# Performance work log

Hardware: AMD Instinct MI355X
Metric: run time of the kernel (lower is better)

Reference implementation:

```python
import jax, jax.numpy as jnp
import numpy as np

N_NODES = 100000


def gcn_conv(x, src, dst, W, b, n):
    # GCNConv: out = D^-1/2 (A + I) D^-1/2 (x @ W) + b, self-loops included in src/dst
    deg = jax.ops.segment_sum(jnp.ones_like(src, dtype=x.dtype), dst, num_segments=n)
    dinv = jnp.where(deg > 0, jax.lax.rsqrt(deg), 0.0)
    norm = dinv[src] * dinv[dst]                      # [E+N]
    h = x @ W                                         # [N, out] small GEMM first (PyG flow)
    msg = h[src] * norm[:, None]                      # gather + scale
    out = jax.ops.segment_sum(msg, dst, num_segments=n)
    return out + b


def setup_inputs() -> dict:
    key = jax.random.key(0)
    k1, k2, k3, k4 = jax.random.split(key, 4)
    F_IN, H, C, E = 128, 16, 4, 3200000
    x = jax.random.normal(k1, (N_NODES, F_IN), dtype=jnp.float32)
    edge_index = jax.random.randint(k2, (2, E), 0, N_NODES, dtype=jnp.int64)
    W1 = jax.random.normal(k3, (F_IN, H), dtype=jnp.float32) * (1.0 / np.sqrt(F_IN))
    b1 = jnp.zeros((H,), dtype=jnp.float32)
    W2 = jax.random.normal(k4, (H, C), dtype=jnp.float32) * (1.0 / np.sqrt(H))
    b2 = jnp.zeros((C,), dtype=jnp.float32)
    return {"x": x, "edge_index": edge_index, "W1": W1, "b1": b1, "W2": W2, "b2": b2}


def reference(x, edge_index, W1, b1, W2, b2):
    n = x.shape[0]
    loop = jnp.arange(n, dtype=edge_index.dtype)
    src = jnp.concatenate([edge_index[0], loop])
    dst = jnp.concatenate([edge_index[1], loop])
    h = gcn_conv(x, src, dst, W1, b1, n)
    h = jax.nn.relu(h)
    # dropout is identity in eval mode
    h = gcn_conv(h, src, dst, W2, b2, n)
    return jax.nn.log_softmax(h, axis=1)
```

## Files before the change

### kernel.cpp

```cpp
#include <hip/hip_runtime.h>
#include <stdint.h>

#define F_IN 128
#define HDIM 16
#define CDIM 4

__global__ void k_detect(const int* __restrict__ w, int* __restrict__ flag) {
    __shared__ int s_any;
    if (threadIdx.x == 0) s_any = 0;
    __syncthreads();
    int nz = 0;
    for (int k = threadIdx.x; k < 1024; k += blockDim.x) nz |= w[2 * k + 1];
    if (nz) atomicOr(&s_any, 1);
    __syncthreads();
    if (threadIdx.x == 0) *flag = (s_any == 0) ? 1 : 0;
}

__global__ void k_zero_deg(int* __restrict__ deg_i, int n) {
    int i = blockIdx.x * blockDim.x + threadIdx.x;
    if (i < n) deg_i[i] = 0;
}

__global__ __launch_bounds__(256) void k_hist(const void* __restrict__ ei,
                                              const int* __restrict__ flag,
                                              int* __restrict__ deg_i, int E) {
    int e = blockIdx.x * blockDim.x + threadIdx.x;
    if (e >= E) return;
    int d;
    if (*flag) d = (int)((const long long*)ei)[E + e];
    else       d = ((const int*)ei)[E + e];
    atomicAdd(&deg_i[d], 1);
}

__global__ __launch_bounds__(256) void k_scan1(const int* __restrict__ deg_i,
                                               int* __restrict__ row_ptr,
                                               int* __restrict__ part, int n) {
    __shared__ int sd[256];
    int base = blockIdx.x * 1024, t = threadIdx.x;
    int v[4], ssum = 0;
#pragma unroll
    for (int k = 0; k < 4; ++k) {
        int i = base + t * 4 + k;
        v[k] = (i < n) ? deg_i[i] : 0;
        ssum += v[k];
    }
    sd[t] = ssum;
    __syncthreads();
    for (int off = 1; off < 256; off <<= 1) {
        int x = (t >= off) ? sd[t - off] : 0;
        __syncthreads();
        sd[t] += x;
        __syncthreads();
    }
    if (t == 255) part[blockIdx.x] = sd[255];
    int run = sd[t] - ssum;
#pragma unroll
    for (int k = 0; k < 4; ++k) {
        int i = base + t * 4 + k;
        if (i < n) row_ptr[i] = run;
        run += v[k];
    }
}

__global__ void k_scan2(int* __restrict__ part, int nb) {
    __shared__ int sd[128];
    int t = threadIdx.x;
    int own = (t < nb) ? part[t] : 0;
    sd[t] = own;
    __syncthreads();
    for (int off = 1; off < 128; off <<= 1) {
        int x = (t >= off) ? sd[t - off] : 0;
        __syncthreads();
        sd[t] += x;
        __syncthreads();
    }
    if (t < nb) part[t] = sd[t] - own;
}

__global__ void k_scan3(int* __restrict__ row_ptr, int* __restrict__ cursor,
                        const int* __restrict__ part, int n, int E) {
    int i = blockIdx.x * blockDim.x + threadIdx.x;
    if (i < n) {
        int r = row_ptr[i] + part[i >> 10];
        row_ptr[i] = r;
        cursor[i] = r;
    }
    if (i == 0) row_ptr[n] = E;
}

__global__ void k_rsqrt(const int* __restrict__ deg_i, float* __restrict__ dinv,
                        int n) {
    int i = blockIdx.x * blockDim.x + threadIdx.x;
    if (i < n) dinv[i] = rsqrtf((float)(deg_i[i] + 1));
}

__global__ __launch_bounds__(256) void k_scatter(const void* __restrict__ ei,
                                                 const int* __restrict__ flag,
                                                 int* __restrict__ cursor,
                                                 int* __restrict__ csr_src, int E) {
    int e = blockIdx.x * blockDim.x + threadIdx.x;
    if (e >= E) return;
    int s, d;
    if (*flag) {
        const long long* q = (const long long*)ei;
        s = (int)q[e]; d = (int)q[E + e];
    } else {
        const int* q = (const int*)ei;
        s = q[e]; d = q[E + e];
    }
    int pos = atomicAdd(&cursor[d], 1);
    csr_src[pos] = s;
}

__global__ __launch_bounds__(256) void k_gemm1(const float* __restrict__ x,
                                               const float* __restrict__ W1,
                                               const float* __restrict__ dinv,
                                               float* __restrict__ h1s, int n) {
    __shared__ float sW[F_IN * HDIM];
    __shared__ float sX[16][F_IN + 4];
    for (int i = threadIdx.x; i < F_IN * HDIM; i += 256) sW[i] = W1[i];
    int row0 = blockIdx.x * 16;
    const float4* x4 = (const float4*)(x + (size_t)row0 * F_IN);
    for (int i = threadIdx.x; i < 512; i += 256) {
        int r = i >> 5, c4 = i & 31;
        if (row0 + r < n) *(float4*)&sX[r][c4 * 4] = x4[i];
    }
    __syncthreads();
    int c = threadIdx.x & 15, r = threadIdx.x >> 4;
    float acc = 0.f;
#pragma unroll
    for (int k = 0; k < F_IN; ++k) acc += sX[r][k] * sW[k * HDIM + c];
    int row = row0 + r;
    if (row < n) h1s[(size_t)row * HDIM + c] = acc * dinv[row];
}

__global__ __launch_bounds__(256) void k_agg1f(const int* __restrict__ row_ptr,
                                               const int* __restrict__ csr_src,
                                               const float* __restrict__ h1s,
                                               const float* __restrict__ dinv,
                                               const float* __restrict__ b1,
                                               const float* __restrict__ W2,
                                               float* __restrict__ h2s, int n) {
    int node = blockIdx.x * 4 + (threadIdx.x >> 6);
    if (node >= n) return;
    int lane = threadIdx.x & 63;
    int f = lane & 15, slot = lane >> 4;
    int start = row_ptr[node], end = row_ptr[node + 1];
    float acc = 0.f;
    for (int j = start + slot; j < end; j += 4)
        acc += h1s[(size_t)csr_src[j] * HDIM + f];
    acc += __shfl_xor(acc, 16, 64);
    acc += __shfl_xor(acc, 32, 64);
    float di = dinv[node];
    float t = fmaxf(di * (acc + h1s[(size_t)node * HDIM + f]) + b1[f], 0.f);
    float4 w2 = ((const float4*)W2)[f];
    float a0 = t * w2.x, a1 = t * w2.y, a2 = t * w2.z, a3 = t * w2.w;
#pragma unroll
    for (int m = 1; m < 16; m <<= 1) {
        a0 += __shfl_xor(a0, m, 64);
        a1 += __shfl_xor(a1, m, 64);
        a2 += __shfl_xor(a2, m, 64);
        a3 += __shfl_xor(a3, m, 64);
    }
    if (lane == 0)
        ((float4*)h2s)[node] = make_float4(a0 * di, a1 * di, a2 * di, a3 * di);
}

__global__ __launch_bounds__(256) void k_agg2f(const int* __restrict__ row_ptr,
                                               const int* __restrict__ csr_src,
                                               const float* __restrict__ h2s,
                                               const float* __restrict__ dinv,
                                               const float* __restrict__ b2,
                                               float* __restrict__ out, int n) {
    int node = blockIdx.x * 4 + (threadIdx.x >> 6);
    if (node >= n) return;
    int lane = threadIdx.x & 63;
    int c = lane & 3, slot = lane >> 2;
    int start = row_ptr[node], end = row_ptr[node + 1];
    float acc = 0.f;
    for (int j = start + slot; j < end; j += 16)
        acc += h2s[(size_t)csr_src[j] * CDIM + c];
#pragma unroll
    for (int m = 4; m < 64; m <<= 1) acc += __shfl_xor(acc, m, 64);
    float z = dinv[node] * (acc + h2s[(size_t)node * CDIM + c]) + b2[c];
    float mx = fmaxf(z, __shfl_xor(z, 1, 64));
    mx = fmaxf(mx, __shfl_xor(mx, 2, 64));
    float ex = __expf(z - mx);
    float ssum = ex + __shfl_xor(ex, 1, 64);
    ssum += __shfl_xor(ssum, 2, 64);
    if (lane < 4) out[(size_t)node * CDIM + c] = z - mx - __logf(ssum);
}

extern "C" void kernel_launch(void* const* d_in, const int* in_sizes, int n_in,
                              void* d_out, int out_size, void* d_ws, size_t ws_size,
                              hipStream_t stream) {
    const float* x  = (const float*)d_in[0];
    const void*  ei = d_in[1];
    const float* W1 = (const float*)d_in[2];
    const float* b1 = (const float*)d_in[3];
    const float* W2 = (const float*)d_in[4];
    const float* b2 = (const float*)d_in[5];
    float* out = (float*)d_out;

    int n = in_sizes[0] / F_IN;
    int E = in_sizes[1] / 2;

    char* ws = (char*)d_ws;
    size_t off = 0;
    auto alloc = [&](size_t bytes) {
        char* p = ws + off;
        off = (off + bytes + 255) & ~(size_t)255;
        return p;
    };
    int*   flag    = (int*)alloc(256);
    int*   deg_i   = (int*)alloc((size_t)n * 4);
    float* dinv    = (float*)alloc((size_t)n * 4);
    int*   row_ptr = (int*)alloc((size_t)(n + 1) * 4);
    int*   cursor  = (int*)alloc((size_t)n * 4);
    int*   part    = (int*)alloc(512 * 4);
    float* h1s     = (float*)alloc((size_t)n * HDIM * 4);
    float* h2s     = (float*)alloc((size_t)n * CDIM * 4);
    int*   csr_src = (int*)alloc((size_t)E * 4);
    (void)ws_size;

    int nb = (n + 1023) / 1024;

    hipLaunchKernelGGL(k_detect, dim3(1), dim3(256), 0, stream, (const int*)ei, flag);
    hipLaunchKernelGGL(k_zero_deg, dim3((n + 255) / 256), dim3(256), 0, stream,
                       deg_i, n);
    hipLaunchKernelGGL(k_hist, dim3((E + 255) / 256), dim3(256), 0, stream,
                       ei, flag, deg_i, E);
    hipLaunchKernelGGL(k_scan1, dim3(nb), dim3(256), 0, stream,
                       deg_i, row_ptr, part, n);
    hipLaunchKernelGGL(k_scan2, dim3(1), dim3(128), 0, stream, part, nb);
    hipLaunchKernelGGL(k_scan3, dim3((n + 255) / 256), dim3(256), 0, stream,
                       row_ptr, cursor, part, n, E);
    hipLaunchKernelGGL(k_rsqrt, dim3((n + 255) / 256), dim3(256), 0, stream,
                       deg_i, dinv, n);
    hipLaunchKernelGGL(k_gemm1, dim3((n + 15) / 16), dim3(256), 0, stream,
                       x, W1, dinv, h1s, n);
    hipLaunchKernelGGL(k_scatter, dim3((E + 255) / 256), dim3(256), 0, stream,
                       ei, flag, cursor, csr_src, E);
    hipLaunchKernelGGL(k_agg1f, dim3((n + 3) / 4), dim3(256), 0, stream,
                       row_ptr, csr_src, h1s, dinv, b1, W2, h2s, n);
    hipLaunchKernelGGL(k_agg2f, dim3((n + 3) / 4), dim3(256), 0, stream,
                       row_ptr, csr_src, h2s, dinv, b2, out, n);
}
```

Baseline: 616.0 us.

## Replace per-node CSR build with coarse bucketed edge sort and shared-memory aggregation

Drops the full per-node CSR construction (global atomic histogram, three-kernel scan, per-edge global atomic scatter). Edges are instead bucketed by destination into groups of 256 nodes, using block-local histograms and tile-level reservation of output ranges. Each edge is packed as source plus a local destination offset. Degree and both aggregation passes then run one block per bucket and accumulate into shared-memory slabs with LDS atomics, which cuts global atomic traffic and kernel count. The trade-off is heavy LDS atomic contention in the aggregation kernels, only about 391 blocks per aggregation launch, and packing limits that assume n below 131072 and at most 512 buckets.

Result: no change. 604.9 us (-1.8%).

```diff
diff --git a/kernel.cpp b/kernel.cpp
--- a/kernel.cpp
+++ b/kernel.cpp
@@ -4,6 +4,10 @@
 #define F_IN 128
 #define HDIM 16
 #define CDIM 4
+#define BSH  8
+#define BNODES 256
+#define SMASK 131071
+#define TILE 8192
 
 __global__ void k_detect(const int* __restrict__ w, int* __restrict__ flag) {
     __shared__ int s_any;
@@ -16,100 +20,104 @@
     if (threadIdx.x == 0) *flag = (s_any == 0) ? 1 : 0;
 }
 
-__global__ void k_zero_deg(int* __restrict__ deg_i, int n) {
-    int i = blockIdx.x * blockDim.x + threadIdx.x;
-    if (i < n) deg_i[i] = 0;
-}
-
-__global__ __launch_bounds__(256) void k_hist(const void* __restrict__ ei,
-                                              const int* __restrict__ flag,
-                                              int* __restrict__ deg_i, int E) {
-    int e = blockIdx.x * blockDim.x + threadIdx.x;
-    if (e >= E) return;
-    int d;
-    if (*flag) d = (int)((const long long*)ei)[E + e];
-    else       d = ((const int*)ei)[E + e];
-    atomicAdd(&deg_i[d], 1);
-}
-
-__global__ __launch_bounds__(256) void k_scan1(const int* __restrict__ deg_i,
-                                               int* __restrict__ row_ptr,
-                                               int* __restrict__ part, int n) {
-    __shared__ int sd[256];
-    int base = blockIdx.x * 1024, t = threadIdx.x;
-    int v[4], ssum = 0;
-#pragma unroll
-    for (int k = 0; k < 4; ++k) {
-        int i = base + t * 4 + k;
-        v[k] = (i < n) ? deg_i[i] : 0;
-        ssum += v[k];
-    }
-    sd[t] = ssum;
-    __syncthreads();
-    for (int off = 1; off < 256; off <<= 1) {
+__global__ void k_zero(int* __restrict__ bcnt) {
+    bcnt[threadIdx.x] = 0;
+}
+
+__global__ __launch_bounds__(256) void k_bhist(const void* __restrict__ ei,
+                                               const int* __restrict__ flag,
+                                               int* __restrict__ bcnt,
+                                               int E, int nbuk) {
+    __shared__ int h[512];
+    for (int b = threadIdx.x; b < 512; b += 256) h[b] = 0;
+    __syncthreads();
+    int stride = gridDim.x * 256;
+    bool f64 = (*flag != 0);
+    for (int e = blockIdx.x * 256 + threadIdx.x; e < E; e += stride) {
+        int d = f64 ? (int)((const long long*)ei)[E + e] : ((const int*)ei)[E + e];
+        atomicAdd(&h[d >> BSH], 1);
+    }
+    __syncthreads();
+    for (int b = threadIdx.x; b < nbuk; b += 256)
+        if (h[b]) atomicAdd(&bcnt[b], h[b]);
+}
+
+__global__ __launch_bounds__(512) void k_bscan(const int* __restrict__ bcnt,
+                                               int* __restrict__ bbase,
+                                               int* __restrict__ bcur,
+                                               int nbuk, int E) {
+    __shared__ int sd[512];
+    int t = threadIdx.x;
+    int own = (t < nbuk) ? bcnt[t] : 0;
+    sd[t] = own;
+    __syncthreads();
+    for (int off = 1; off < 512; off <<= 1) {
         int x = (t >= off) ? sd[t - off] : 0;
         __syncthreads();
         sd[t] += x;
         __syncthreads();
     }
-    if (t == 255) part[blockIdx.x] = sd[255];
-    int run = sd[t] - ssum;
-#pragma unroll
-    for (int k = 0; k < 4; ++k) {
-        int i = base + t * 4 + k;
-        if (i < n) row_ptr[i] = run;
-        run += v[k];
-    }
-}
-
-__global__ void k_scan2(int* __restrict__ part, int nb) {
-    __shared__ int sd[128];
-    int t = threadIdx.x;
-    int own = (t < nb) ? part[t] : 0;
-    sd[t] = own;
-    __syncthreads();
-    for (int off = 1; off < 128; off <<= 1) {
-        int x = (t >= off) ? sd[t - off] : 0;
-        __syncthreads();
-        sd[t] += x;
-        __syncthreads();
-    }
-    if (t < nb) part[t] = sd[t] - own;
-}
-
-__global__ void k_scan3(int* __restrict__ row_ptr, int* __restrict__ cursor,
-                        const int* __restrict__ part, int n, int E) {
-    int i = blockIdx.x * blockDim.x + threadIdx.x;
-    if (i < n) {
-        int r = row_ptr[i] + part[i >> 10];
-        row_ptr[i] = r;
-        cursor[i] = r;
-    }
-    if (i == 0) row_ptr[n] = E;
-}
-
-__global__ void k_rsqrt(const int* __restrict__ deg_i, float* __restrict__ dinv,
-                        int n) {
-    int i = blockIdx.x * blockDim.x + threadIdx.x;
-    if (i < n) dinv[i] = rsqrtf((float)(deg_i[i] + 1));
-}
-
-__global__ __launch_bounds__(256) void k_scatter(const void* __restrict__ ei,
-                                                 const int* __restrict__ flag,
-                                                 int* __restrict__ cursor,
-                                                 int* __restrict__ csr_src, int E) {
-    int e = blockIdx.x * blockDim.x + threadIdx.x;
-    if (e >= E) return;
-    int s, d;
-    if (*flag) {
-        const long long* q = (const long long*)ei;
-        s = (int)q[e]; d = (int)q[E + e];
-    } else {
-        const int* q = (const int*)ei;
-        s = q[e]; d = q[E + e];
-    }
-    int pos = atomicAdd(&cursor[d], 1);
-    csr_src[pos] = s;
+    if (t < nbuk) { int ex = sd[t] - own; bbase[t] = ex; bcur[t] = ex; }
+    if (t == 0) bbase[nbuk] = E;
+}
+
+__global__ __launch_bounds__(512) void k_bscatter(const void* __restrict__ ei,
+                                                  const int* __restrict__ flag,
+                                                  int* __restrict__ bcur,
+                                                  int* __restrict__ bpk,
+                                                  int E, int nbuk) {
+    __shared__ int hist[512], loff[512], rbase[512];
+    __shared__ int lpk[TILE];
+    __shared__ unsigned short lb[TILE];
+    int tid = threadIdx.x;
+    int tstart = blockIdx.x * TILE;
+    int cnt = min(TILE, E - tstart);
+    for (int b = tid; b < 512; b += 512) { hist[b] = 0; loff[b] = 0; }
+    __syncthreads();
+    bool f64 = (*flag != 0);
+    for (int k = 0; k < TILE / 512; ++k) {
+        int i = tid + k * 512;
+        if (i < cnt) {
+            int e = tstart + i, s, d;
+            if (f64) {
+                const long long* q = (const long long*)ei;
+                s = (int)q[e]; d = (int)q[E + e];
+            } else {
+                const int* q = (const int*)ei;
+                s = q[e]; d = q[E + e];
+            }
+            int b = d >> BSH;
+            lpk[i] = s | ((d & (BNODES - 1)) << 17);
+            lb[i] = (unsigned short)b;
+            atomicAdd(&hist[b], 1);
+        }
+    }
+    __syncthreads();
+    if (tid < nbuk && hist[tid] > 0) rbase[tid] = atomicAdd(&bcur[tid], hist[tid]);
+    __syncthreads();
+    for (int k = 0; k < TILE / 512; ++k) {
+        int i = tid + k * 512;
+        if (i < cnt) {
+            int b = lb[i];
+            int p = rbase[b] + atomicAdd(&loff[b], 1);
+            bpk[p] = lpk[i];
+        }
+    }
+}
+
+__global__ __launch_bounds__(256) void k_bdeg(const int* __restrict__ bbase,
+                                              const int* __restrict__ bpk,
+                                              float* __restrict__ dinv, int n) {
+    __shared__ int cnt[BNODES];
+    int b = blockIdx.x, tid = threadIdx.x;
+    cnt[tid] = 0;
+    __syncthreads();
+    int start = bbase[b], end = bbase[b + 1];
+    for (int i = start + tid; i < end; i += 256)
+        atomicAdd(&cnt[bpk[i] >> 17], 1);
+    __syncthreads();
+    int g = b * BNODES + tid;
+    if (g < n) dinv[g] = rsqrtf((float)(cnt[tid] + 1));
 }
 
 __global__ __launch_bounds__(256) void k_gemm1(const float* __restrict__ x,
@@ -134,61 +142,91 @@
     if (row < n) h1s[(size_t)row * HDIM + c] = acc * dinv[row];
 }
 
-__global__ __launch_bounds__(256) void k_agg1f(const int* __restrict__ row_ptr,
-                                               const int* __restrict__ csr_src,
+__global__ __launch_bounds__(512) void k_bagg1(const int* __restrict__ bbase,
+                                               const int* __restrict__ bpk,
                                                const float* __restrict__ h1s,
                                                const float* __restrict__ dinv,
                                                const float* __restrict__ b1,
                                                const float* __restrict__ W2,
                                                float* __restrict__ h2s, int n) {
-    int node = blockIdx.x * 4 + (threadIdx.x >> 6);
-    if (node >= n) return;
-    int lane = threadIdx.x & 63;
-    int f = lane & 15, slot = lane >> 4;
-    int start = row_ptr[node], end = row_ptr[node + 1];
-    float acc = 0.f;
-    for (int j = start + slot; j < end; j += 4)
-        acc += h1s[(size_t)csr_src[j] * HDIM + f];
-    acc += __shfl_xor(acc, 16, 64);
-    acc += __shfl_xor(acc, 32, 64);
-    float di = dinv[node];
-    float t = fmaxf(di * (acc + h1s[(size_t)node * HDIM + f]) + b1[f], 0.f);
-    float4 w2 = ((const float4*)W2)[f];
-    float a0 = t * w2.x, a1 = t * w2.y, a2 = t * w2.z, a3 = t * w2.w;
+    __shared__ float slab[BNODES * HDIM];
+    int b = blockIdx.x, tid = threadIdx.x;
+    for (int j = tid; j < BNODES * HDIM; j += 512) slab[j] = 0.f;
+    __syncthreads();
+    int start = bbase[b], end = bbase[b + 1];
+    int f = tid & 15;
+    int i = start + (tid >> 4);
+    for (; i + 32 < end; i += 64) {
+        int e0 = bpk[i], e1 = bpk[i + 32];
+        float v0 = h1s[(size_t)(e0 & SMASK) * HDIM + f];
+        float v1 = h1s[(size_t)(e1 & SMASK) * HDIM + f];
+        atomicAdd(&slab[(e0 >> 17) * HDIM + f], v0);
+        atomicAdd(&slab[(e1 >> 17) * HDIM + f], v1);
+    }
+    for (; i < end; i += 32) {
+        int e0 = bpk[i];
+        float v0 = h1s[(size_t)(e0 & SMASK) * HDIM + f];
+        atomicAdd(&slab[(e0 >> 17) * HDIM + f], v0);
+    }
+    __syncthreads();
+    if (tid < BNODES) {
+        int g = b * BNODES + tid;
+        if (g < n) {
+            float di = dinv[g];
+            float a0 = 0.f, a1 = 0.f, a2 = 0.f, a3 = 0.f;
 #pragma unroll
-    for (int m = 1; m < 16; m <<= 1) {
-        a0 += __shfl_xor(a0, m, 64);
-        a1 += __shfl_xor(a1, m, 64);
-        a2 += __shfl_xor(a2, m, 64);
-        a3 += __shfl_xor(a3, m, 64);
-    }
-    if (lane == 0)
-        ((float4*)h2s)[node] = make_float4(a0 * di, a1 * di, a2 * di, a3 * di);
-}
-
-__global__ __launch_bounds__(256) void k_agg2f(const int* __restrict__ row_ptr,
-                                               const int* __restrict__ csr_src,
+            for (int j = 0; j < HDIM; ++j) {
+                float t = fmaxf(di * (slab[tid * HDIM + j] +
+                                      h1s[(size_t)g * HDIM + j]) + b1[j], 0.f);
+                float4 w2 = ((const float4*)W2)[j];
+                a0 += t * w2.x; a1 += t * w2.y; a2 += t * w2.z; a3 += t * w2.w;
+            }
+            ((float4*)h2s)[g] = make_float4(a0 * di, a1 * di, a2 * di, a3 * di);
+        }
+    }
+}
+
+__global__ __launch_bounds__(512) void k_bagg2(const int* __restrict__ bbase,
+                                               const int* __restrict__ bpk,
                                                const float* __restrict__ h2s,
                                                const float* __restrict__ dinv,
                                                const float* __restrict__ b2,
                                                float* __restrict__ out, int n) {
-    int node = blockIdx.x * 4 + (threadIdx.x >> 6);
-    if (node >= n) return;
-    int lane = threadIdx.x & 63;
-    int c = lane & 3, slot = lane >> 2;
-    int start = row_ptr[node], end = row_ptr[node + 1];
-    float acc = 0.f;
-    for (int j = start + slot; j < end; j += 16)
-        acc += h2s[(size_t)csr_src[j] * CDIM + c];
-#pragma unroll
-    for (int m = 4; m < 64; m <<= 1) acc += __shfl_xor(acc, m, 64);
-    float z = dinv[node] * (acc + h2s[(size_t)node * CDIM + c]) + b2[c];
-    float mx = fmaxf(z, __shfl_xor(z, 1, 64));
-    mx = fmaxf(mx, __shfl_xor(mx, 2, 64));
-    float ex = __expf(z - mx);
-    float ssum = ex + __shfl_xor(ex, 1, 64);
-    ssum += __shfl_xor(ssum, 2, 64);
-    if (lane < 4) out[(size_t)node * CDIM + c] = z - mx - __logf(ssum);
+    __shared__ float slab[BNODES * CDIM];
+    int b = blockIdx.x, tid = threadIdx.x;
+    for (int j = tid; j < BNODES * CDIM; j += 512) slab[j] = 0.f;
+    __syncthreads();
+    int start = bbase[b], end = bbase[b + 1];
+    int c = tid & 3;
+    int i = start + (tid >> 2);
+    for (; i + 128 < end; i += 256) {
+        int e0 = bpk[i], e1 = bpk[i + 128];
+        float v0 = h2s[(size_t)(e0 & SMASK) * CDIM + c];
+        float v1 = h2s[(size_t)(e1 & SMASK) * CDIM + c];
+        atomicAdd(&slab[(e0 >> 17) * CDIM + c], v0);
+        atomicAdd(&slab[(e1 >> 17) * CDIM + c], v1);
+    }
+    for (; i < end; i += 128) {
+        int e0 = bpk[i];
+        float v0 = h2s[(size_t)(e0 & SMASK) * CDIM + c];
+        atomicAdd(&slab[(e0 >> 17) * CDIM + c], v0);
+    }
+    __syncthreads();
+    if (tid < BNODES) {
+        int g = b * BNODES + tid;
+        if (g < n) {
+            float di = dinv[g];
+            float4 hs = ((const float4*)h2s)[g];
+            float z0 = di * (slab[tid * 4 + 0] + hs.x) + b2[0];
+            float z1 = di * (slab[tid * 4 + 1] + hs.y) + b2[1];
+            float z2 = di * (slab[tid * 4 + 2] + hs.z) + b2[2];
+            float z3 = di * (slab[tid * 4 + 3] + hs.w) + b2[3];
+            float m = fmaxf(fmaxf(z0, z1), fmaxf(z2, z3));
+            float s = expf(z0 - m) + expf(z1 - m) + expf(z2 - m) + expf(z3 - m);
+            float l = m + logf(s);
+            ((float4*)out)[g] = make_float4(z0 - l, z1 - l, z2 - l, z3 - l);
+        }
+    }
 }
 
 extern "C" void kernel_launch(void* const* d_in, const int* in_sizes, int n_in,
@@ -204,6 +242,7 @@
 
     int n = in_sizes[0] / F_IN;
     int E = in_sizes[1] / 2;
+    int nbuk = (n + BNODES - 1) >> BSH;
 
     char* ws = (char*)d_ws;
     size_t off = 0;
@@ -212,37 +251,31 @@
         off = (off + bytes + 255) & ~(size_t)255;
         return p;
     };
-    int*   flag    = (int*)alloc(256);
-    int*   deg_i   = (int*)alloc((size_t)n * 4);
-    float* dinv    = (float*)alloc((size_t)n * 4);
-    int*   row_ptr = (int*)alloc((size_t)(n + 1) * 4);
-    int*   cursor  = (int*)alloc((size_t)n * 4);
-    int*   part    = (int*)alloc(512 * 4);
-    float* h1s     = (float*)alloc((size_t)n * HDIM * 4);
-    float* h2s     = (float*)alloc((size_t)n * CDIM * 4);
-    int*   csr_src = (int*)alloc((size_t)E * 4);
+    int*   flag  = (int*)alloc(256);
+    int*   bcnt  = (int*)alloc(512 * 4);
+    int*   bbase = (int*)alloc(513 * 4);
+    int*   bcur  = (int*)alloc(512 * 4);
+    float* dinv  = (float*)alloc((size_t)n * 4);
+    float* h1s   = (float*)alloc((size_t)n * HDIM * 4);
+    float* h2s   = (float*)alloc((size_t)n * CDIM * 4);
+    int*   bpk   = (int*)alloc((size_t)E * 4);
     (void)ws_size;
 
-    int nb = (n + 1023) / 1024;
+    int ntiles = (E + TILE - 1) / TILE;
 
     hipLaunchKernelGGL(k_detect, dim3(1), dim3(256), 0, stream, (const int*)ei, flag);
-    hipLaunchKernelGGL(k_zero_deg, dim3((n + 255) / 256), dim3(256), 0, stream,
-                       deg_i, n);
-    hipLaunchKernelGGL(k_hist, dim3((E + 255) / 256), dim3(256), 0, stream,
-                       ei, flag, deg_i, E);
-    hipLaunchKernelGGL(k_scan1, dim3(nb), dim3(256), 0, stream,
-                       deg_i, row_ptr, part, n);
-    hipLaunchKernelGGL(k_scan2, dim3(1), dim3(128), 0, stream, part, nb);
-    hipLaunchKernelGGL(k_scan3, dim3((n + 255) / 256), dim3(256), 0, stream,
-                       row_ptr, cursor, part, n, E);
-    hipLaunchKernelGGL(k_rsqrt, dim3((n + 255) / 256), dim3(256), 0, stream,
-                       deg_i, dinv, n);
+    hipLaunchKernelGGL(k_zero, dim3(1), dim3(512), 0, stream, bcnt);
+    hipLaunchKernelGGL(k_bhist, dim3(256), dim3(256), 0, stream,
+                       ei, flag, bcnt, E, nbuk);
+    hipLaunchKernelGGL(k_bscan, dim3(1), dim3(512), 0, stream, bcnt, bbase, bcur,
+                       nbuk, E);
+    hipLaunchKernelGGL(k_bscatter, dim3(ntiles), dim3(512), 0, stream,
+                       ei, flag, bcur, bpk, E, nbuk);
+    hipLaunchKernelGGL(k_bdeg, dim3(nbuk), dim3(256), 0, stream, bbase, bpk, dinv, n);
     hipLaunchKernelGGL(k_gemm1, dim3((n + 15) / 16), dim3(256), 0, stream,
                        x, W1, dinv, h1s, n);
-    hipLaunchKernelGGL(k_scatter, dim3((E + 255) / 256), dim3(256), 0, stream,
-                       ei, flag, cursor, csr_src, E);
-    hipLaunchKernelGGL(k_agg1f, dim3((n + 3) / 4), dim3(256), 0, stream,
-                       row_ptr, csr_src, h1s, dinv, b1, W2, h2s, n);
-    hipLaunchKernelGGL(k_agg2f, dim3((n + 3) / 4), dim3(256), 0, stream,
-                       row_ptr, csr_src, h2s, dinv, b2, out, n);
-}
+    hipLaunchKernelGGL(k_bagg1, dim3(nbuk), dim3(512), 0, stream,
+                       bbase, bpk, h1s, dinv, b1, W2, h2s, n);
+    hipLaunchKernelGGL(k_bagg2, dim3(nbuk), dim3(512), 0, stream,
+                       bbase, bpk, h2s, dinv, b2, out, n);
+}
```
